# Kernel tuning notes

Measured on AMD Instinct MI355X. Metric: run time of the kernel, lower is better.

The kernel has to match this reference:

```python
import jax, jax.numpy as jnp
import numpy as np

B, S, H = 64, 256, 768
T, D = 13, 64  # ent_type_size, inner_dim
NEG = 1e12


def setup_inputs() -> dict:
    key = jax.random.key(0)
    k1, k2 = jax.random.split(key)
    return {
        "last_hidden_state": jax.random.normal(k1, (B, S, H), dtype=jnp.float32),
        "dense_w": jax.random.normal(k2, (H, T * 2 * D), dtype=jnp.float32) * (1.0 / np.sqrt(H)),
        "dense_b": jnp.zeros((T * 2 * D,), dtype=jnp.float32),
        "attention_mask": jnp.ones((B, S), dtype=jnp.float32),
    }


def _rope_sin_cos(seq_len, dim, dtype):
    # sinusoidal_position_embedding: even slots sin, odd slots cos
    pos = jnp.arange(seq_len, dtype=dtype)[:, None]                      # [S,1]
    inv = jnp.power(10000.0, -2.0 * jnp.arange(dim // 2, dtype=dtype) / dim)
    ang = pos * inv                                                      # [S,D/2]
    # cos_pos = emb[...,1::2].repeat_interleave(2) ; sin_pos = emb[...,::2].repeat_interleave(2)
    cos_pos = jnp.repeat(jnp.cos(ang), 2, axis=-1)                       # [S,D]
    sin_pos = jnp.repeat(jnp.sin(ang), 2, axis=-1)                       # [S,D]
    return sin_pos, cos_pos


def _rotate(x):
    # stack([-x[...,1::2], x[...,::2]], -1).reshape(x.shape)
    x2 = jnp.stack([-x[..., 1::2], x[..., ::2]], axis=-1)
    return x2.reshape(x.shape)


def reference(last_hidden_state, dense_w, dense_b, attention_mask):
    b, s, _ = last_hidden_state.shape
    out = last_hidden_state @ dense_w + dense_b                          # [B,S,T*2D]
    out = out.reshape(b, s, T, 2 * D)                                    # split+stack
    qw, kw = out[..., :D], out[..., D:]                                  # [B,S,T,D]

    sin_pos, cos_pos = _rope_sin_cos(s, D, out.dtype)
    cosb = cos_pos[None, :, None, :]                                     # [1,S,1,D]
    sinb = sin_pos[None, :, None, :]
    qw = qw * cosb + _rotate(qw) * sinb
    kw = kw * cosb + _rotate(kw) * sinb

    logits = jnp.einsum('bmhd,bnhd->bhmn', qw, kw)                       # [B,T,S,S]

    pad = attention_mask[:, None, None, :]                               # mask over key dim n
    logits = logits * pad - (1.0 - pad) * NEG
    tril = jnp.tril(jnp.ones((s, s), dtype=logits.dtype), -1)            # strict lower tri
    logits = logits - tril * NEG
    return logits / (D ** 0.5)
```

## Files before the change

### kernel.cpp

```cpp
#include <hip/hip_runtime.h>

#define S_LEN 256
#define H_DIM 768
#define T_HEADS 13
#define WN 1664
#define NEGV 1.0e12f

typedef __bf16 bf16x8 __attribute__((ext_vector_type(8)));
typedef float f32x4 __attribute__((ext_vector_type(4)));
typedef float f32x16 __attribute__((ext_vector_type(16)));
typedef unsigned int u32x4 __attribute__((ext_vector_type(4)));
typedef int i32x8 __attribute__((ext_vector_type(8)));

static __device__ __forceinline__ ushort f2bf(float x) {
  unsigned u = __float_as_uint(x);
  return (ushort)((u + 0x7FFFu + ((u >> 16) & 1u)) >> 16);
}

#define GLOAD16(gp, lp)                                                        \
  __builtin_amdgcn_global_load_lds(                                            \
      (const __attribute__((address_space(1))) unsigned int*)(gp),             \
      (__attribute__((address_space(3))) unsigned int*)(lp), 16, 0, 0)

#define PREP_LHS_BLOCKS 6144
#define PREP_WT_BLOCKS 312
#define PREP_ROPE_BLOCKS 16

__global__ __launch_bounds__(256) void prep_all(const float* __restrict__ lhs,
                                                const float* __restrict__ W,
                                                unsigned char* __restrict__ lhs8,
                                                unsigned char* __restrict__ wt8,
                                                float2* __restrict__ rope) {
  const int tid = threadIdx.x;
  const unsigned bx = blockIdx.x;
  if (bx < PREP_LHS_BLOCKS) {
    size_t base = ((size_t)bx * 256 + tid) * 8;
    float4 v0 = *reinterpret_cast<const float4*>(lhs + base);
    float4 v1 = *reinterpret_cast<const float4*>(lhs + base + 4);
    int d0 = __builtin_amdgcn_cvt_pk_fp8_f32(v0.x, v0.y, 0, false);
    d0 = __builtin_amdgcn_cvt_pk_fp8_f32(v0.z, v0.w, d0, true);
    int d1 = __builtin_amdgcn_cvt_pk_fp8_f32(v1.x, v1.y, 0, false);
    d1 = __builtin_amdgcn_cvt_pk_fp8_f32(v1.z, v1.w, d1, true);
    uint2 u = make_uint2((unsigned)d0, (unsigned)d1);
    *reinterpret_cast<uint2*>(lhs8 + base) = u;
    return;
  }
  if (bx < PREP_LHS_BLOCKS + PREP_WT_BLOCKS) {
    __shared__ float T[64][68];
    const int blk = bx - PREP_LHS_BLOCKS;
    const int k0 = (blk % 12) * 64, c0 = (blk / 12) * 64;
#pragma unroll
    for (int p = 0; p < 4; ++p) {
      int f = p * 256 + tid;
      int r = f >> 4, cg = f & 15;
      float4 v = *reinterpret_cast<const float4*>(W + (size_t)(k0 + r) * WN + c0 + cg * 4);
      T[r][cg * 4 + 0] = v.x; T[r][cg * 4 + 1] = v.y;
      T[r][cg * 4 + 2] = v.z; T[r][cg * 4 + 3] = v.w;
    }
    __syncthreads();
    const int orow = tid >> 2, kq = tid & 3;
    float tf[16];
#pragma unroll
    for (int j = 0; j < 16; ++j) tf[j] = T[kq * 16 + j][orow];
    int d[4];
#pragma unroll
    for (int q = 0; q < 4; ++q) {
      d[q] = __builtin_amdgcn_cvt_pk_fp8_f32(tf[q * 4], tf[q * 4 + 1], 0, false);
      d[q] = __builtin_amdgcn_cvt_pk_fp8_f32(tf[q * 4 + 2], tf[q * 4 + 3], d[q], true);
    }
    uint4 u = make_uint4((unsigned)d[0], (unsigned)d[1], (unsigned)d[2], (unsigned)d[3]);
    *reinterpret_cast<uint4*>(wt8 + (size_t)(c0 + orow) * H_DIM + k0 + kq * 16) = u;
    return;
  }
  const int blk = bx - (PREP_LHS_BLOCKS + PREP_WT_BLOCKS);
  const int row = blk * 16 + (tid >> 4);
  const int cq = (tid & 15) * 4;
#pragma unroll
  for (int q = 0; q < 4; ++q) {
    int c = cq + q;
    float inv = exp2f(-(float)(c >> 1) * 0.4152410118609203f);
    float sv, cv;
    __sincosf((float)row * inv, &sv, &cv);
    rope[(size_t)row * 64 + c] = make_float2(cv, sv);
  }
}

static __device__ __forceinline__ i32x8 frag8(const unsigned char* base, int row,
                                              int ks, int hi2, int l31) {
  union { u32x4 h[2]; i32x8 v; } u;
  const int u0 = (ks * 4 + hi2 * 2 + 0) ^ (l31 & 7);
  const int u1 = (ks * 4 + hi2 * 2 + 1) ^ (l31 & 7);
  u.h[0] = *reinterpret_cast<const u32x4*>(base + row * 128 + u0 * 16);
  u.h[1] = *reinterpret_cast<const u32x4*>(base + row * 128 + u1 * 16);
  return u.v;
}

__global__ __launch_bounds__(256, 2) void gp_fused(
    const unsigned char* __restrict__ lhs8, const unsigned char* __restrict__ wt8,
    const float* __restrict__ bias, const float2* __restrict__ rope,
    const float* __restrict__ amask, float* __restrict__ out) {
  const int x = blockIdx.x;
  const int xcd = x & 7;
  const int seq = x >> 3;
  const int grp = seq / 52;
  const int loc = seq % 52;
  const int b = (xcd + 8 * grp) * 4 + loc / 13;
  const int th = loc % 13;
  const int bid = b * T_HEADS + th;
  const int tid = threadIdx.x;
  const int w = tid >> 6;
  const int lane = tid & 63;
  const int l31 = lane & 31;
  const int hi2 = lane >> 5;
  const int lr8 = lane >> 3;
  const int lsu = (lane & 7) ^ lr8;

  __shared__ union {
    struct { unsigned char A[256 * 128]; unsigned char W[128 * 128]; } p1;
    struct { ushort Q[256][72]; ushort K[256][72]; } p2;
  } sm;

  const unsigned char* Ag = lhs8 + (size_t)b * S_LEN * H_DIM;
  const unsigned char* Wg = wt8 + (size_t)th * 128 * H_DIM;

  f32x16 c2[2][4];
#pragma unroll
  for (int mt = 0; mt < 2; ++mt)
#pragma unroll
    for (int ni = 0; ni < 4; ++ni) c2[mt][ni] = (f32x16){};

  for (int k0 = 0; k0 < H_DIM; k0 += 128) {
#pragma unroll
    for (int j = 0; j < 8; ++j) {
      const int r0 = w * 64 + j * 8;
      GLOAD16(Ag + (size_t)(r0 + lr8) * H_DIM + k0 + lsu * 16, &sm.p1.A[r0 * 128]);
    }
#pragma unroll
    for (int j = 0; j < 4; ++j) {
      const int r0 = w * 32 + j * 8;
      GLOAD16(Wg + (size_t)(r0 + lr8) * H_DIM + k0 + lsu * 16, &sm.p1.W[r0 * 128]);
    }
    __syncthreads();
#pragma unroll
    for (int ks = 0; ks < 2; ++ks) {
#pragma unroll
      for (int mt = 0; mt < 2; ++mt) {
        i32x8 a = frag8(sm.p1.A, w * 64 + mt * 32 + l31, ks, hi2, l31);
#pragma unroll
        for (int ni = 0; ni < 4; ++ni) {
          i32x8 bb = frag8(sm.p1.W, ni * 32 + l31, ks, hi2, l31);
          c2[mt][ni] = __builtin_amdgcn_mfma_scale_f32_32x32x64_f8f6f4(
              a, bb, c2[mt][ni], 0, 0, 0, 0x7F, 0, 0x7F);
        }
      }
    }
    __syncthreads();
  }

  float bj2[4];
#pragma unroll
  for (int ni = 0; ni < 4; ++ni) bj2[ni] = bias[th * 128 + ni * 32 + l31];
  const float sgn = (l31 & 1) ? 1.0f : -1.0f;

#pragma unroll
  for (int mt = 0; mt < 2; ++mt) {
#pragma unroll
    for (int reg = 0; reg < 16; ++reg) {
      int ml = w * 64 + mt * 32 + (reg & 3) + 8 * (reg >> 2) + 4 * hi2;
#pragma unroll
      for (int ni = 0; ni < 2; ++ni) {
        float2 cs = rope[(size_t)ml * 64 + ni * 32 + l31];
        {
          float v = c2[mt][ni][reg] + bj2[ni];
          float o = __shfl_xor(v, 1);
          sm.p2.Q[ml][ni * 32 + l31] = f2bf(v * cs.x + sgn * o * cs.y);
        }
        {
          float v = c2[mt][ni + 2][reg] + bj2[ni + 2];
          float o = __shfl_xor(v, 1);
          sm.p2.K[ml][ni * 32 + l31] = f2bf(v * cs.x + sgn * o * cs.y);
        }
      }
    }
  }
  __syncthreads();

  bf16x8 qf2[2][4];
#pragma unroll
  for (int mtile = 0; mtile < 2; ++mtile)
#pragma unroll
    for (int ks = 0; ks < 4; ++ks)
      qf2[mtile][ks] = *reinterpret_cast<const bf16x8*>(
          &sm.p2.Q[w * 64 + mtile * 32 + l31][ks * 16 + hi2 * 8]);

  const size_t outbase = (size_t)bid * (S_LEN * (size_t)S_LEN);
#pragma unroll 1
  for (int nt = 0; nt < 8; ++nt) {
    bf16x8 kf2[4];
#pragma unroll
    for (int ks = 0; ks < 4; ++ks)
      kf2[ks] = *reinterpret_cast<const bf16x8*>(
          &sm.p2.K[nt * 32 + l31][ks * 16 + hi2 * 8]);

    const int ncol = nt * 32 + l31;
    const float pad = amask[b * S_LEN + ncol];
    const float sub = (1.0f - pad) * NEGV;

#pragma unroll
    for (int mtile = 0; mtile < 2; ++mtile) {
      f32x16 cq = {};
#pragma unroll
      for (int ks = 0; ks < 4; ++ks)
        cq = __builtin_amdgcn_mfma_f32_32x32x16_bf16(qf2[mtile][ks], kf2[ks], cq, 0, 0, 0);

#pragma unroll
      for (int reg = 0; reg < 16; ++reg) {
        int m = w * 64 + mtile * 32 + (reg & 3) + 8 * (reg >> 2) + 4 * hi2;
        float v = cq[reg] * pad - sub;
        if (m > ncol) v -= NEGV;
        __builtin_nontemporal_store(v * 0.125f, &out[outbase + (size_t)m * S_LEN + ncol]);
      }
    }
  }
}

__global__ __launch_bounds__(256, 1) void gp_fallback(
    const float* __restrict__ lhs, const float* __restrict__ Wd,
    const float* __restrict__ bias, const float* __restrict__ amask,
    float* __restrict__ out) {
  const int bid0 = blockIdx.x;
  const int bid = (bid0 & 7) * 104 + (bid0 >> 3);
  const int b = bid / T_HEADS;
  const int th = bid % T_HEADS;
  const int wcol0 = th * 128;
  const int tid = threadIdx.x;
  const int w = tid >> 6;
  const int lane = tid & 63;
  const int lo = lane & 15;
  const int hi = lane >> 4;
  const int l31 = lane & 31;
  const int hi2 = lane >> 5;

  __shared__ union {
    struct { ushort A[256][72]; ushort W[128][72]; } p1;
    struct { ushort Q[256][72]; ushort K[256][72]; } p2;
  } sm;
  __shared__ float mask_s[256];

  mask_s[tid] = amask[b * S_LEN + tid];

  f32x4 acc[4][8];
#pragma unroll
  for (int mi = 0; mi < 4; ++mi)
#pragma unroll
    for (int ni = 0; ni < 8; ++ni) acc[mi][ni] = (f32x4){0.f, 0.f, 0.f, 0.f};

  const float* Ab = lhs + (size_t)b * (S_LEN * H_DIM);
  const int wc4 = tid & 31, wrg = tid >> 5;
  for (int k0 = 0; k0 < H_DIM; k0 += 64) {
#pragma unroll
    for (int p = 0; p < 16; ++p) {
      int f = p * 256 + tid;
      int m = f >> 4, c4 = f & 15;
      float4 v = *reinterpret_cast<const float4*>(Ab + (size_t)m * H_DIM + k0 + c4 * 4);
      *reinterpret_cast<ushort4*>(&sm.p1.A[m][c4 * 4]) =
          make_ushort4(f2bf(v.x), f2bf(v.y), f2bf(v.z), f2bf(v.w));
    }
    {
      ushort wt[8][4];
#pragma unroll
      for (int r8 = 0; r8 < 8; ++r8) {
        float4 v = *reinterpret_cast<const float4*>(
            Wd + (size_t)(k0 + wrg * 8 + r8) * WN + wcol0 + wc4 * 4);
        wt[r8][0] = f2bf(v.x); wt[r8][1] = f2bf(v.y);
        wt[r8][2] = f2bf(v.z); wt[r8][3] = f2bf(v.w);
      }
#pragma unroll
      for (int cc = 0; cc < 4; ++cc) {
        *reinterpret_cast<ushort4*>(&sm.p1.W[wc4 * 4 + cc][wrg * 8]) =
            make_ushort4(wt[0][cc], wt[1][cc], wt[2][cc], wt[3][cc]);
        *reinterpret_cast<ushort4*>(&sm.p1.W[wc4 * 4 + cc][wrg * 8 + 4]) =
            make_ushort4(wt[4][cc], wt[5][cc], wt[6][cc], wt[7][cc]);
      }
    }
    __syncthreads();
#pragma unroll
    for (int kk = 0; kk < 2; ++kk) {
      bf16x8 af[4];
#pragma unroll
      for (int mi = 0; mi < 4; ++mi)
        af[mi] = *reinterpret_cast<const bf16x8*>(&sm.p1.A[w * 64 + mi * 16 + lo][kk * 32 + hi * 8]);
#pragma unroll
      for (int ni = 0; ni < 8; ++ni) {
        bf16x8 bfr = *reinterpret_cast<const bf16x8*>(&sm.p1.W[ni * 16 + lo][kk * 32 + hi * 8]);
#pragma unroll
        for (int mi = 0; mi < 4; ++mi)
          acc[mi][ni] = __builtin_amdgcn_mfma_f32_16x16x32_bf16(af[mi], bfr, acc[mi][ni], 0, 0, 0);
      }
    }
    __syncthreads();
  }

  float bj[8];
#pragma unroll
  for (int ni = 0; ni < 8; ++ni) bj[ni] = bias[wcol0 + ni * 16 + lo];

  float inv_[4];
#pragma unroll
  for (int ii = 0; ii < 4; ++ii)
    inv_[ii] = exp2f(-(float)(ii * 8 + (lo >> 1)) * 0.4152410118609203f);
  const float sgn = (lo & 1) ? 1.0f : -1.0f;

#pragma unroll
  for (int mi = 0; mi < 4; ++mi) {
#pragma unroll
    for (int r = 0; r < 4; ++r) {
      int m = w * 64 + mi * 16 + hi * 4 + r;
#pragma unroll
      for (int ii = 0; ii < 4; ++ii) {
        float sv, cv;
        __sincosf((float)m * inv_[ii], &sv, &cv);
        {
          float v = acc[mi][ii][r] + bj[ii];
          float o = __shfl_xor(v, 1);
          sm.p2.Q[m][ii * 16 + lo] = f2bf(v * cv + sgn * o * sv);
        }
        {
          float v = acc[mi][ii + 4][r] + bj[ii + 4];
          float o = __shfl_xor(v, 1);
          sm.p2.K[m][ii * 16 + lo] = f2bf(v * cv + sgn * o * sv);
        }
      }
    }
  }
  __syncthreads();

  bf16x8 qf2[2][4];
#pragma unroll
  for (int mtile = 0; mtile < 2; ++mtile)
#pragma unroll
    for (int ks = 0; ks < 4; ++ks)
      qf2[mtile][ks] = *reinterpret_cast<const bf16x8*>(
          &sm.p2.Q[w * 64 + mtile * 32 + l31][ks * 16 + hi2 * 8]);

  const size_t outbase = (size_t)bid * (S_LEN * (size_t)S_LEN);
#pragma unroll 1
  for (int nt = 0; nt < 8; ++nt) {
    bf16x8 kf2[4];
#pragma unroll
    for (int ks = 0; ks < 4; ++ks)
      kf2[ks] = *reinterpret_cast<const bf16x8*>(
          &sm.p2.K[nt * 32 + l31][ks * 16 + hi2 * 8]);

    const int ncol = nt * 32 + l31;
    const float pad = mask_s[ncol];
    const float sub = (1.0f - pad) * NEGV;

#pragma unroll
    for (int mtile = 0; mtile < 2; ++mtile) {
      f32x16 cq = {};
#pragma unroll
      for (int ks = 0; ks < 4; ++ks)
        cq = __builtin_amdgcn_mfma_f32_32x32x16_bf16(qf2[mtile][ks], kf2[ks], cq, 0, 0, 0);

#pragma unroll
      for (int reg = 0; reg < 16; ++reg) {
        int m = w * 64 + mtile * 32 + (reg & 3) + 8 * (reg >> 2) + 4 * hi2;
        float v = cq[reg] * pad - sub;
        if (m > ncol) v -= NEGV;
        __builtin_nontemporal_store(v * 0.125f, &out[outbase + (size_t)m * S_LEN + ncol]);
      }
    }
  }
}

extern "C" void kernel_launch(void* const* d_in, const int* in_sizes, int n_in,
                              void* d_out, int out_size, void* d_ws, size_t ws_size,
                              hipStream_t stream) {
  const float* lhs = (const float*)d_in[0];
  const float* Wd = (const float*)d_in[1];
  const float* bias = (const float*)d_in[2];
  const float* amask = (const float*)d_in[3];
  float* out = (float*)d_out;

  const size_t rope_bytes = (size_t)256 * 64 * sizeof(float2);
  const size_t lhs8_bytes = (size_t)64 * S_LEN * H_DIM;
  const size_t wt8_bytes = (size_t)WN * H_DIM;
  const size_t need = rope_bytes + lhs8_bytes + wt8_bytes;

  if (ws_size >= need) {
    float2* rope = (float2*)d_ws;
    unsigned char* lhs8 = (unsigned char*)d_ws + rope_bytes;
    unsigned char* wt8 = lhs8 + lhs8_bytes;
    prep_all<<<dim3(PREP_LHS_BLOCKS + PREP_WT_BLOCKS + PREP_ROPE_BLOCKS), 256, 0, stream>>>(
        lhs, Wd, lhs8, wt8, rope);
    gp_fused<<<dim3(64 * T_HEADS), 256, 0, stream>>>(lhs8, wt8, bias, rope, amask, out);
  } else {
    gp_fallback<<<dim3(64 * T_HEADS), 256, 0, stream>>>(lhs, Wd, bias, amask, out);
  }
}
```

Baseline: 82.92 us.

## Double-buffer GEMM staging and split work across eight waves per block

Doubles threads per block to 512, with each wave handling 32 rows instead of 64, and double-buffers the fp8 A/W tiles in LDS. The next K tile is prefetched while MFMAs run on the current one. This is meant to hide global-to-LDS load latency and halve per-wave accumulator registers. The larger LDS footprint likely reduces resident blocks per CU.

Result: slower. 89.62 us (+8.1%).

```diff
diff --git a/kernel.cpp b/kernel.cpp
--- a/kernel.cpp
+++ b/kernel.cpp
@@ -95,7 +95,7 @@
   return u.v;
 }
 
-__global__ __launch_bounds__(256, 2) void gp_fused(
+__global__ __launch_bounds__(512, 2) void gp_fused(
     const unsigned char* __restrict__ lhs8, const unsigned char* __restrict__ wt8,
     const float* __restrict__ bias, const float2* __restrict__ rope,
     const float* __restrict__ amask, float* __restrict__ out) {
@@ -116,45 +116,52 @@
   const int lsu = (lane & 7) ^ lr8;
 
   __shared__ union {
-    struct { unsigned char A[256 * 128]; unsigned char W[128 * 128]; } p1;
+    unsigned char stage[2][49152];
     struct { ushort Q[256][72]; ushort K[256][72]; } p2;
   } sm;
 
   const unsigned char* Ag = lhs8 + (size_t)b * S_LEN * H_DIM;
   const unsigned char* Wg = wt8 + (size_t)th * 128 * H_DIM;
 
-  f32x16 c2[2][4];
-#pragma unroll
-  for (int mt = 0; mt < 2; ++mt)
-#pragma unroll
-    for (int ni = 0; ni < 4; ++ni) c2[mt][ni] = (f32x16){};
-
-  for (int k0 = 0; k0 < H_DIM; k0 += 128) {
-#pragma unroll
-    for (int j = 0; j < 8; ++j) {
-      const int r0 = w * 64 + j * 8;
-      GLOAD16(Ag + (size_t)(r0 + lr8) * H_DIM + k0 + lsu * 16, &sm.p1.A[r0 * 128]);
-    }
-#pragma unroll
-    for (int j = 0; j < 4; ++j) {
-      const int r0 = w * 32 + j * 8;
-      GLOAD16(Wg + (size_t)(r0 + lr8) * H_DIM + k0 + lsu * 16, &sm.p1.W[r0 * 128]);
+  f32x16 c2[4];
+#pragma unroll
+  for (int ni = 0; ni < 4; ++ni) c2[ni] = (f32x16){};
+
+#define STAGE_TILE(t, buf)                                                         \
+  do {                                                                             \
+    unsigned char* sb_ = sm.stage[buf];                                            \
+    _Pragma("unroll") for (int j = 0; j < 4; ++j) {                                \
+      const int r0 = w * 32 + j * 8;                                               \
+      GLOAD16(Ag + (size_t)(r0 + lr8) * H_DIM + (t) * 128 + lsu * 16,              \
+              sb_ + r0 * 128);                                                     \
+    }                                                                              \
+    _Pragma("unroll") for (int j = 0; j < 2; ++j) {                                \
+      const int r0 = w * 16 + j * 8;                                               \
+      GLOAD16(Wg + (size_t)(r0 + lr8) * H_DIM + (t) * 128 + lsu * 16,              \
+              sb_ + 32768 + r0 * 128);                                             \
+    }                                                                              \
+  } while (0)
+
+  STAGE_TILE(0, 0);
+  __syncthreads();
+  int cur = 0;
+#pragma unroll 1
+  for (int t = 0; t < 6; ++t) {
+    if (t + 1 < 6) STAGE_TILE(t + 1, cur ^ 1);
+    const unsigned char* sa = sm.stage[cur];
+    const unsigned char* sw = sm.stage[cur] + 32768;
+#pragma unroll
+    for (int ks = 0; ks < 2; ++ks) {
+      i32x8 a = frag8(sa, w * 32 + l31, ks, hi2, l31);
+#pragma unroll
+      for (int ni = 0; ni < 4; ++ni) {
+        i32x8 bb = frag8(sw, ni * 32 + l31, ks, hi2, l31);
+        c2[ni] = __builtin_amdgcn_mfma_scale_f32_32x32x64_f8f6f4(
+            a, bb, c2[ni], 0, 0, 0, 0x7F, 0, 0x7F);
+      }
     }
     __syncthreads();
-#pragma unroll
-    for (int ks = 0; ks < 2; ++ks) {
-#pragma unroll
-      for (int mt = 0; mt < 2; ++mt) {
-        i32x8 a = frag8(sm.p1.A, w * 64 + mt * 32 + l31, ks, hi2, l31);
-#pragma unroll
-        for (int ni = 0; ni < 4; ++ni) {
-          i32x8 bb = frag8(sm.p1.W, ni * 32 + l31, ks, hi2, l31);
-          c2[mt][ni] = __builtin_amdgcn_mfma_scale_f32_32x32x64_f8f6f4(
-              a, bb, c2[mt][ni], 0, 0, 0, 0x7F, 0, 0x7F);
-        }
-      }
-    }
-    __syncthreads();
+    cur ^= 1;
   }
 
   float bj2[4];
@@ -163,35 +170,30 @@
   const float sgn = (l31 & 1) ? 1.0f : -1.0f;
 
 #pragma unroll
-  for (int mt = 0; mt < 2; ++mt) {
-#pragma unroll
-    for (int reg = 0; reg < 16; ++reg) {
-      int ml = w * 64 + mt * 32 + (reg & 3) + 8 * (reg >> 2) + 4 * hi2;
-#pragma unroll
-      for (int ni = 0; ni < 2; ++ni) {
-        float2 cs = rope[(size_t)ml * 64 + ni * 32 + l31];
-        {
-          float v = c2[mt][ni][reg] + bj2[ni];
-          float o = __shfl_xor(v, 1);
-          sm.p2.Q[ml][ni * 32 + l31] = f2bf(v * cs.x + sgn * o * cs.y);
-        }
-        {
-          float v = c2[mt][ni + 2][reg] + bj2[ni + 2];
-          float o = __shfl_xor(v, 1);
-          sm.p2.K[ml][ni * 32 + l31] = f2bf(v * cs.x + sgn * o * cs.y);
-        }
+  for (int reg = 0; reg < 16; ++reg) {
+    int ml = w * 32 + (reg & 3) + 8 * (reg >> 2) + 4 * hi2;
+#pragma unroll
+    for (int ni = 0; ni < 2; ++ni) {
+      float2 cs = rope[(size_t)ml * 64 + ni * 32 + l31];
+      {
+        float v = c2[ni][reg] + bj2[ni];
+        float o = __shfl_xor(v, 1);
+        sm.p2.Q[ml][ni * 32 + l31] = f2bf(v * cs.x + sgn * o * cs.y);
+      }
+      {
+        float v = c2[ni + 2][reg] + bj2[ni + 2];
+        float o = __shfl_xor(v, 1);
+        sm.p2.K[ml][ni * 32 + l31] = f2bf(v * cs.x + sgn * o * cs.y);
       }
     }
   }
   __syncthreads();
 
-  bf16x8 qf2[2][4];
-#pragma unroll
-  for (int mtile = 0; mtile < 2; ++mtile)
-#pragma unroll
-    for (int ks = 0; ks < 4; ++ks)
-      qf2[mtile][ks] = *reinterpret_cast<const bf16x8*>(
-          &sm.p2.Q[w * 64 + mtile * 32 + l31][ks * 16 + hi2 * 8]);
+  bf16x8 qf2[4];
+#pragma unroll
+  for (int ks = 0; ks < 4; ++ks)
+    qf2[ks] = *reinterpret_cast<const bf16x8*>(
+        &sm.p2.Q[w * 32 + l31][ks * 16 + hi2 * 8]);
 
   const size_t outbase = (size_t)bid * (S_LEN * (size_t)S_LEN);
 #pragma unroll 1
@@ -206,20 +208,17 @@
     const float pad = amask[b * S_LEN + ncol];
     const float sub = (1.0f - pad) * NEGV;
 
-#pragma unroll
-    for (int mtile = 0; mtile < 2; ++mtile) {
-      f32x16 cq = {};
-#pragma unroll
-      for (int ks = 0; ks < 4; ++ks)
-        cq = __builtin_amdgcn_mfma_f32_32x32x16_bf16(qf2[mtile][ks], kf2[ks], cq, 0, 0, 0);
-
-#pragma unroll
-      for (int reg = 0; reg < 16; ++reg) {
-        int m = w * 64 + mtile * 32 + (reg & 3) + 8 * (reg >> 2) + 4 * hi2;
-        float v = cq[reg] * pad - sub;
-        if (m > ncol) v -= NEGV;
-        __builtin_nontemporal_store(v * 0.125f, &out[outbase + (size_t)m * S_LEN + ncol]);
-      }
+    f32x16 cq = {};
+#pragma unroll
+    for (int ks = 0; ks < 4; ++ks)
+      cq = __builtin_amdgcn_mfma_f32_32x32x16_bf16(qf2[ks], kf2[ks], cq, 0, 0, 0);
+
+#pragma unroll
+    for (int reg = 0; reg < 16; ++reg) {
+      int m = w * 32 + (reg & 3) + 8 * (reg >> 2) + 4 * hi2;
+      float v = cq[reg] * pad - sub;
+      if (m > ncol) v -= NEGV;
+      __builtin_nontemporal_store(v * 0.125f, &out[outbase + (size_t)m * S_LEN + ncol]);
     }
   }
 }
@@ -394,7 +393,7 @@
     unsigned char* wt8 = lhs8 + lhs8_bytes;
     prep_all<<<dim3(PREP_LHS_BLOCKS + PREP_WT_BLOCKS + PREP_ROPE_BLOCKS), 256, 0, stream>>>(
         lhs, Wd, lhs8, wt8, rope);
-    gp_fused<<<dim3(64 * T_HEADS), 256, 0, stream>>>(lhs8, wt8, bias, rope, amask, out);
+    gp_fused<<<dim3(64 * T_HEADS), 512, 0, stream>>>(lhs8, wt8, bias, rope, amask, out);
   } else {
     gp_fallback<<<dim3(64 * T_HEADS), 256, 0, stream>>>(lhs, Wd, bias, amask, out);
   }
```
